# Kernel optimization log

Measured on AMD Instinct MI355X. Metric: run time of the kernel, lower is better.

The kernel has to match this reference:

```python
import jax, jax.numpy as jnp
import numpy as np


def setup_inputs() -> dict:
    key = jax.random.key(0)
    k1, k2 = jax.random.split(key)
    N, B, C, D, H, W = 20, 4, 1, 8, 128, 128
    forecasts = jax.random.normal(k1, (N, B, C, D, H, W), dtype=jnp.float32)
    observations = jax.random.normal(k2, (B, C, D, H, W), dtype=jnp.float32)
    return {"forecasts": forecasts, "observations": observations}


def reference(forecasts, observations):
    # CRPS ~= (1/N) sum_i |x_i - y| - (1/(2 N^2)) sum_ij |x_i - x_j|
    # forecasts: (N, B, C, D, H, W); observations: (B, C, D, H, W)
    first_term = jnp.mean(jnp.abs(forecasts - observations[None]), axis=0)
    # pairwise |x_i - x_j| over the ensemble axis -> mean over (i, j), halved
    pairwise = jnp.abs(forecasts[:, None] - forecasts[None, :])  # (N, N, B, C, D, H, W)
    second_term = jnp.mean(pairwise, axis=(0, 1)) * 0.5
    crps = first_term - second_term  # (B, C, D, H, W)
    return jnp.mean(crps)  # reduction='mean'
```

## Files before the change

### kernel.cpp

```cpp
#include <hip/hip_runtime.h>
#include <hip/hip_bf16.h>


constexpr int N_ENS = 20;

typedef float f4 __attribute__((ext_vector_type(4)));

__global__ __launch_bounds__(256) void crps_partial_v4(
    const f4* __restrict__ fc,
    const f4* __restrict__ obs,
    const float* __restrict__ fc_s,
    const float* __restrict__ obs_s,
    float* __restrict__ partial,
    int nv, int P)
{
    const int stride = gridDim.x * blockDim.x;
    const int gtid = blockIdx.x * blockDim.x + threadIdx.x;
    float local = 0.0f;

    for (int v = gtid; v < nv; v += stride) {
        f4 x[N_ENS];
        #pragma unroll
        for (int i = 0; i < N_ENS; ++i)
            x[i] = fc[(size_t)i * (size_t)nv + (size_t)v];
        const f4 y = obs[v];

        #pragma unroll
        for (int c = 0; c < 4; ++c) {
            float xc[N_ENS];
            #pragma unroll
            for (int i = 0; i < N_ENS; ++i) xc[i] = x[i][c];
            const float yc = y[c];

            float t1 = 0.0f;
            #pragma unroll
            for (int i = 0; i < N_ENS; ++i) t1 += fabsf(xc[i] - yc);

            float t2 = 0.0f;
            #pragma unroll
            for (int i = 0; i < N_ENS; ++i) {
                #pragma unroll
                for (int j = i + 1; j < N_ENS; ++j)
                    t2 += fabsf(xc[i] - xc[j]);
            }
            local += t1 * (1.0f / N_ENS) - t2 * (1.0f / (N_ENS * N_ENS));
        }
    }

    for (int p = 4 * nv + gtid; p < P; p += stride) {
        float xc[N_ENS];
        #pragma unroll
        for (int i = 0; i < N_ENS; ++i) xc[i] = fc_s[(size_t)i * (size_t)P + p];
        const float yc = obs_s[p];
        float t1 = 0.0f, t2 = 0.0f;
        #pragma unroll
        for (int i = 0; i < N_ENS; ++i) t1 += fabsf(xc[i] - yc);
        #pragma unroll
        for (int i = 0; i < N_ENS; ++i) {
            #pragma unroll
            for (int j = i + 1; j < N_ENS; ++j)
                t2 += fabsf(xc[i] - xc[j]);
        }
        local += t1 * (1.0f / N_ENS) - t2 * (1.0f / (N_ENS * N_ENS));
    }

    #pragma unroll
    for (int off = 32; off > 0; off >>= 1)
        local += __shfl_down(local, off, 64);

    __shared__ float wsum[4];
    const int lane = threadIdx.x & 63;
    const int wid  = threadIdx.x >> 6;
    if (lane == 0) wsum[wid] = local;
    __syncthreads();
    if (threadIdx.x == 0)
        partial[blockIdx.x] = wsum[0] + wsum[1] + wsum[2] + wsum[3];
}

__global__ __launch_bounds__(256) void crps_reduce_kernel(
    const float* __restrict__ partial,
    int nblocks,
    float* __restrict__ out,
    float inv_total)
{
    double s = 0.0;
    for (int i = threadIdx.x; i < nblocks; i += blockDim.x)
        s += (double)partial[i];

    #pragma unroll
    for (int off = 32; off > 0; off >>= 1)
        s += __shfl_down(s, off, 64);

    __shared__ double wsum[4];
    const int lane = threadIdx.x & 63;
    const int wid  = threadIdx.x >> 6;
    if (lane == 0) wsum[wid] = s;
    __syncthreads();
    if (threadIdx.x == 0) {
        double tot = wsum[0] + wsum[1] + wsum[2] + wsum[3];
        out[0] = (float)(tot * (double)inv_total);
    }
}

extern "C" void kernel_launch(void* const* d_in, const int* in_sizes, int n_in,
                              void* d_out, int out_size, void* d_ws, size_t ws_size,
                              hipStream_t stream) {
    const float* fc  = (const float*)d_in[0];
    const float* obs = (const float*)d_in[1];
    float* out = (float*)d_out;

    const int P  = in_sizes[1];
    const int nv = P >> 2;

    const int block = 256;
    int nblocks = (nv + block - 1) / block;
    if (nblocks < 1) nblocks = 1;
    if (nblocks > 4096) nblocks = 4096;

    float* partial = (float*)d_ws;

    crps_partial_v4<<<nblocks, block, 0, stream>>>(
        (const f4*)fc, (const f4*)obs, fc, obs, partial, nv, P);
    crps_reduce_kernel<<<1, block, 0, stream>>>(partial, nblocks, out, 1.0f / (float)P);
}
```

Measured before the change: 19.33 us.

## Fuse partial and final reduction into one cooperative kernel with grid sync

```diff
diff --git a/kernel.cpp b/kernel.cpp
--- a/kernel.cpp
+++ b/kernel.cpp
@@ -1,17 +1,21 @@
 #include <hip/hip_runtime.h>
 #include <hip/hip_bf16.h>
+#include <hip/hip_cooperative_groups.h>
+
+namespace cg = cooperative_groups;
 
 
 constexpr int N_ENS = 20;
 
 typedef float f4 __attribute__((ext_vector_type(4)));
 
-__global__ __launch_bounds__(256) void crps_partial_v4(
+__global__ __launch_bounds__(256) void crps_coop(
     const f4* __restrict__ fc,
     const f4* __restrict__ obs,
     const float* __restrict__ fc_s,
     const float* __restrict__ obs_s,
     float* __restrict__ partial,
+    float* __restrict__ out,
     int nv, int P)
 {
     const int stride = gridDim.x * blockDim.x;
@@ -22,8 +26,8 @@
         f4 x[N_ENS];
         #pragma unroll
         for (int i = 0; i < N_ENS; ++i)
-            x[i] = fc[(size_t)i * (size_t)nv + (size_t)v];
-        const f4 y = obs[v];
+            x[i] = __builtin_nontemporal_load(&fc[(size_t)i * (size_t)nv + (size_t)v]);
+        const f4 y = __builtin_nontemporal_load(&obs[v]);
 
         #pragma unroll
         for (int c = 0; c < 4; ++c) {
@@ -73,32 +77,29 @@
     const int wid  = threadIdx.x >> 6;
     if (lane == 0) wsum[wid] = local;
     __syncthreads();
-    if (threadIdx.x == 0)
+    if (threadIdx.x == 0) {
         partial[blockIdx.x] = wsum[0] + wsum[1] + wsum[2] + wsum[3];
-}
+        __threadfence();
+    }
 
-__global__ __launch_bounds__(256) void crps_reduce_kernel(
-    const float* __restrict__ partial,
-    int nblocks,
-    float* __restrict__ out,
-    float inv_total)
-{
-    double s = 0.0;
-    for (int i = threadIdx.x; i < nblocks; i += blockDim.x)
-        s += (double)partial[i];
+    cg::this_grid().sync();
 
-    #pragma unroll
-    for (int off = 32; off > 0; off >>= 1)
-        s += __shfl_down(s, off, 64);
+    if (blockIdx.x == 0) {
+        double s = 0.0;
+        for (int i = threadIdx.x; i < (int)gridDim.x; i += blockDim.x)
+            s += (double)partial[i];
 
-    __shared__ double wsum[4];
-    const int lane = threadIdx.x & 63;
-    const int wid  = threadIdx.x >> 6;
-    if (lane == 0) wsum[wid] = s;
-    __syncthreads();
-    if (threadIdx.x == 0) {
-        double tot = wsum[0] + wsum[1] + wsum[2] + wsum[3];
-        out[0] = (float)(tot * (double)inv_total);
+        #pragma unroll
+        for (int off = 32; off > 0; off >>= 1)
+            s += __shfl_down(s, off, 64);
+
+        __shared__ double dsum[4];
+        if (lane == 0) dsum[wid] = s;
+        __syncthreads();
+        if (threadIdx.x == 0) {
+            double tot = dsum[0] + dsum[1] + dsum[2] + dsum[3];
+            out[0] = (float)(tot / (double)P);
+        }
     }
 }
 
@@ -109,17 +110,23 @@
     const float* obs = (const float*)d_in[1];
     float* out = (float*)d_out;
 
-    const int P  = in_sizes[1];
-    const int nv = P >> 2;
+    int P  = in_sizes[1];
+    int nv = P >> 2;
 
     const int block = 256;
     int nblocks = (nv + block - 1) / block;
     if (nblocks < 1) nblocks = 1;
-    if (nblocks > 4096) nblocks = 4096;
+    if (nblocks > 512) nblocks = 512;
 
     float* partial = (float*)d_ws;
 
-    crps_partial_v4<<<nblocks, block, 0, stream>>>(
-        (const f4*)fc, (const f4*)obs, fc, obs, partial, nv, P);
-    crps_reduce_kernel<<<1, block, 0, stream>>>(partial, nblocks, out, 1.0f / (float)P);
+    const f4* fc4  = (const f4*)fc;
+    const f4* obs4 = (const f4*)obs;
+
+    void* args[] = { (void*)&fc4, (void*)&obs4, (void*)&fc, (void*)&obs,
+                     (void*)&partial, (void*)&out, (void*)&nv, (void*)&P };
+
+    hipLaunchCooperativeKernel((const void*)crps_coop,
+                               dim3(nblocks), dim3(block),
+                               args, 0, stream);
 }
```

Result: slower. 71.48 us (+269.7%).

## Fuse final reduction into main kernel via last-block atomic counter

Applied to the files above, without the earlier changes.

```diff
diff --git a/kernel.cpp b/kernel.cpp
--- a/kernel.cpp
+++ b/kernel.cpp
@@ -6,13 +6,15 @@
 
 typedef float f4 __attribute__((ext_vector_type(4)));
 
-__global__ __launch_bounds__(256) void crps_partial_v4(
+__global__ __launch_bounds__(256) void crps_fused(
     const f4* __restrict__ fc,
     const f4* __restrict__ obs,
     const float* __restrict__ fc_s,
     const float* __restrict__ obs_s,
     float* __restrict__ partial,
-    int nv, int P)
+    unsigned* __restrict__ counter,
+    float* __restrict__ out,
+    int nv, int P, int nblocks)
 {
     const int stride = gridDim.x * blockDim.x;
     const int gtid = blockIdx.x * blockDim.x + threadIdx.x;
@@ -69,36 +71,38 @@
         local += __shfl_down(local, off, 64);
 
     __shared__ float wsum[4];
+    __shared__ int winner;
     const int lane = threadIdx.x & 63;
     const int wid  = threadIdx.x >> 6;
     if (lane == 0) wsum[wid] = local;
     __syncthreads();
-    if (threadIdx.x == 0)
-        partial[blockIdx.x] = wsum[0] + wsum[1] + wsum[2] + wsum[3];
-}
+    if (threadIdx.x == 0) {
+        float bsum = wsum[0] + wsum[1] + wsum[2] + wsum[3];
+        __hip_atomic_store(&partial[blockIdx.x], bsum,
+                           __ATOMIC_RELEASE, __HIP_MEMORY_SCOPE_AGENT);
+        unsigned old = __hip_atomic_fetch_add(counter, 1u,
+                           __ATOMIC_ACQ_REL, __HIP_MEMORY_SCOPE_AGENT);
+        winner = ((old % (unsigned)nblocks) == (unsigned)(nblocks - 1));
+    }
+    __syncthreads();
 
-__global__ __launch_bounds__(256) void crps_reduce_kernel(
-    const float* __restrict__ partial,
-    int nblocks,
-    float* __restrict__ out,
-    float inv_total)
-{
-    double s = 0.0;
-    for (int i = threadIdx.x; i < nblocks; i += blockDim.x)
-        s += (double)partial[i];
+    if (winner) {
+        double s = 0.0;
+        for (int i = threadIdx.x; i < nblocks; i += blockDim.x)
+            s += (double)__hip_atomic_load(&partial[i],
+                           __ATOMIC_ACQUIRE, __HIP_MEMORY_SCOPE_AGENT);
 
-    #pragma unroll
-    for (int off = 32; off > 0; off >>= 1)
-        s += __shfl_down(s, off, 64);
+        #pragma unroll
+        for (int off = 32; off > 0; off >>= 1)
+            s += __shfl_down(s, off, 64);
 
-    __shared__ double wsum[4];
-    const int lane = threadIdx.x & 63;
-    const int wid  = threadIdx.x >> 6;
-    if (lane == 0) wsum[wid] = s;
-    __syncthreads();
-    if (threadIdx.x == 0) {
-        double tot = wsum[0] + wsum[1] + wsum[2] + wsum[3];
-        out[0] = (float)(tot * (double)inv_total);
+        __shared__ double dsum[4];
+        if (lane == 0) dsum[wid] = s;
+        __syncthreads();
+        if (threadIdx.x == 0) {
+            double tot = dsum[0] + dsum[1] + dsum[2] + dsum[3];
+            out[0] = (float)(tot / (double)P);
+        }
     }
 }
 
@@ -113,13 +117,15 @@
     const int nv = P >> 2;
 
     const int block = 256;
-    int nblocks = (nv + block - 1) / block;
-    if (nblocks < 1) nblocks = 1;
-    if (nblocks > 4096) nblocks = 4096;
+    int want = (nv + block - 1) / block;
+    if (want < 1) want = 1;
+    int nblocks = 1;
+    while (nblocks * 2 <= want && nblocks < 512) nblocks *= 2;
 
-    float* partial = (float*)d_ws;
+    unsigned* counter = (unsigned*)d_ws;
+    float* partial = (float*)((char*)d_ws + 128);
 
-    crps_partial_v4<<<nblocks, block, 0, stream>>>(
-        (const f4*)fc, (const f4*)obs, fc, obs, partial, nv, P);
-    crps_reduce_kernel<<<1, block, 0, stream>>>(partial, nblocks, out, 1.0f / (float)P);
+    crps_fused<<<nblocks, block, 0, stream>>>(
+        (const f4*)fc, (const f4*)obs, fc, obs,
+        partial, counter, out, nv, P, nblocks);
 }
```

Result: slower. 25.24 us (+30.6%).
